# Performance work log

Hardware: AMD Instinct MI355X
Metric: run time of the kernel (lower is better)

## Reference

```python
import jax, jax.numpy as jnp
import numpy as np

B, TV, L = 64, 80, 20
V, H, VD = 10000, 512, 4096
NH = 4  # attention heads


def _lstm_layer(x, wih, whh, bih, bhh):
    # x: [B, T, H_in]; PyTorch gate order i, f, g, o
    b, t = x.shape[0], x.shape[1]
    h_dim = whh.shape[1]
    xg = jnp.einsum('bti,gi->btg', x, wih) + bih + bhh  # [B, T, 4H]

    def step(carry, xg_t):
        h, c = carry
        g = xg_t + h @ whh.T
        i, f, gg, o = jnp.split(g, 4, axis=-1)
        c = jax.nn.sigmoid(f) * c + jax.nn.sigmoid(i) * jnp.tanh(gg)
        h = jax.nn.sigmoid(o) * jnp.tanh(c)
        return (h, c), h

    h0 = jnp.zeros((b, h_dim), x.dtype)
    _, hs = jax.lax.scan(step, (h0, h0), jnp.swapaxes(xg, 0, 1))
    return jnp.swapaxes(hs, 0, 1)


def _lstm2(x, p0, p1):
    # 2-layer LSTM, eval mode (dropout=0.2 between layers is identity at eval)
    return _lstm_layer(_lstm_layer(x, *p0), *p1)


def _mha(q, kv, in_w, in_b, out_w, out_b):
    # torch nn.MultiheadAttention, batch_first, self/cross attention
    h = q.shape[-1]
    d = h // NH
    wq, wk, wv = jnp.split(in_w, 3, axis=0)
    bq, bk, bv = jnp.split(in_b, 3, axis=0)
    Q = (q @ wq.T + bq).reshape(q.shape[0], q.shape[1], NH, d)
    K = (kv @ wk.T + bk).reshape(kv.shape[0], kv.shape[1], NH, d)
    Vv = (kv @ wv.T + bv).reshape(kv.shape[0], kv.shape[1], NH, d)
    scale = jnp.asarray(1.0 / np.sqrt(d), q.dtype)
    scores = jnp.einsum('bqhd,bkhd->bhqk', Q, K) * scale
    attn = jax.nn.softmax(scores, axis=-1)
    out = jnp.einsum('bhqk,bkhd->bqhd', attn, Vv).reshape(q.shape[0], q.shape[1], h)
    return out @ out_w.T + out_b


def setup_inputs() -> dict:
    key = jax.random.key(0)
    ks = iter(jax.random.split(key, 40))
    s = 0.05
    d = {}
    d['video_features'] = jax.random.normal(next(ks), (B, TV, VD), jnp.float32)
    d['captions'] = jax.random.randint(next(ks), (B, L), 0, V, jnp.int64)
    d['vpw'] = jax.random.normal(next(ks), (H, VD), jnp.float32) * s
    d['vpb'] = jnp.zeros((H,), jnp.float32)
    d['emb_table'] = jax.random.normal(next(ks), (V, H), jnp.float32) * s
    for pfx in ['e0', 'e1', 'd0', 'd1']:
        d[pfx + '_wih'] = jax.random.normal(next(ks), (4 * H, H), jnp.float32) * s
        d[pfx + '_whh'] = jax.random.normal(next(ks), (4 * H, H), jnp.float32) * s
        d[pfx + '_bih'] = jnp.zeros((4 * H,), jnp.float32)
        d[pfx + '_bhh'] = jnp.zeros((4 * H,), jnp.float32)
    d['a_inw'] = jax.random.normal(next(ks), (3 * H, H), jnp.float32) * s
    d['a_inb'] = jnp.zeros((3 * H,), jnp.float32)
    d['a_outw'] = jax.random.normal(next(ks), (H, H), jnp.float32) * s
    d['a_outb'] = jnp.zeros((H,), jnp.float32)
    d['ow'] = jax.random.normal(next(ks), (V, H), jnp.float32) * s
    d['ob'] = jnp.zeros((V,), jnp.float32)
    return d


def reference(video_features, captions, vpw, vpb, emb_table,
              e0_wih, e0_whh, e0_bih, e0_bhh, e1_wih, e1_whh, e1_bih, e1_bhh,
              d0_wih, d0_whh, d0_bih, d0_bhh, d1_wih, d1_whh, d1_bih, d1_bhh,
              a_inw, a_inb, a_outw, a_outb, ow, ob):
    # Encoder
    vproj = jnp.einsum('btv,hv->bth', video_features, vpw) + vpb
    enc = _lstm2(vproj, (e0_wih, e0_whh, e0_bih, e0_bhh), (e1_wih, e1_whh, e1_bih, e1_bhh))
    # Decoder (teacher forcing, sampling_prob=0): inputs are captions[:, :-1].
    # Each step's attention query only sees encoder output -> vectorize over steps.
    emb = emb_table[captions[:, :-1]]                      # [B, L-1, H]
    attended = _mha(emb, enc, a_inw, a_inb, a_outw, a_outb)  # [B, L-1, H]
    dec = _lstm2(attended, (d0_wih, d0_whh, d0_bih, d0_bhh), (d1_wih, d1_whh, d1_bih, d1_bhh))
    logits = jnp.einsum('bth,vh->btv', dec, ow) + ob       # [B, L-1, V]
    return logits
```

## Files before the change

### kernel.cpp

```cpp
#include <hip/hip_runtime.h>
#include <hip/hip_bf16.h>
#include <math.h>

typedef unsigned short ushort_t;
typedef __attribute__((ext_vector_type(8))) short short8;
typedef __attribute__((ext_vector_type(4))) float f32x4;

#define B_ 64
#define TV_ 80
#define TD_ 19
#define H_ 512
#define VD_ 4096
#define NV_ 10000
#define G4_ 2048
#define HN_ 32768
#define XN_ 16384

__device__ __forceinline__ float bf2f(ushort_t u) {
  unsigned int x = ((unsigned int)u) << 16;
  float f;
  __builtin_memcpy(&f, &x, 4);
  return f;
}
__device__ __forceinline__ ushort_t f2bf(float f) {
  unsigned int x;
  __builtin_memcpy(&x, &f, 4);
  x = (x + 0x7FFFu + ((x >> 16) & 1u)) >> 16;
  return (ushort_t)x;
}
__device__ __forceinline__ float sigmoidf_(float x) { return 1.0f / (1.0f + expf(-x)); }
__device__ __forceinline__ short8 zero8() {
  short8 z = {0, 0, 0, 0, 0, 0, 0, 0};
  return z;
}
__device__ __forceinline__ short8 cvt_frag(const float* __restrict__ p) {
  float4 v0 = *reinterpret_cast<const float4*>(p);
  float4 v1 = *reinterpret_cast<const float4*>(p + 4);
  short8 r;
  r[0] = (short)f2bf(v0.x); r[1] = (short)f2bf(v0.y);
  r[2] = (short)f2bf(v0.z); r[3] = (short)f2bf(v0.w);
  r[4] = (short)f2bf(v1.x); r[5] = (short)f2bf(v1.y);
  r[6] = (short)f2bf(v1.z); r[7] = (short)f2bf(v1.w);
  return r;
}
__device__ __forceinline__ short8 unpack_hi(uint4 q0, uint4 q1) {
  union { unsigned int u[4]; short8 s; } r;
  r.u[0] = __builtin_amdgcn_perm(q0.y, q0.x, 0x05040100u);
  r.u[1] = __builtin_amdgcn_perm(q0.w, q0.z, 0x05040100u);
  r.u[2] = __builtin_amdgcn_perm(q1.y, q1.x, 0x05040100u);
  r.u[3] = __builtin_amdgcn_perm(q1.w, q1.z, 0x05040100u);
  return r.s;
}
__device__ __forceinline__ short8 unpack_lo(uint4 q0, uint4 q1) {
  union { unsigned int u[4]; short8 s; } r;
  r.u[0] = __builtin_amdgcn_perm(q0.y, q0.x, 0x07060302u);
  r.u[1] = __builtin_amdgcn_perm(q0.w, q0.z, 0x07060302u);
  r.u[2] = __builtin_amdgcn_perm(q1.y, q1.x, 0x07060302u);
  r.u[3] = __builtin_amdgcn_perm(q1.w, q1.z, 0x07060302u);
  return r.s;
}

__global__ __launch_bounds__(256) void cvt_f32_bf16(const float* __restrict__ in,
                                                    ushort_t* __restrict__ outp, int n4) {
  int i = blockIdx.x * 256 + threadIdx.x;
  if (i < n4) {
    float4 v = reinterpret_cast<const float4*>(in)[i];
    ushort4 r;
    r.x = f2bf(v.x); r.y = f2bf(v.y); r.z = f2bf(v.z); r.w = f2bf(v.w);
    reinterpret_cast<ushort4*>(outp)[i] = r;
  }
}

__device__ __forceinline__ void cvt_blk(const float* __restrict__ in,
                                        ushort_t* __restrict__ outp, int local, int tid) {
  int i = local * 256 + tid;
  float4 v = reinterpret_cast<const float4*>(in)[i];
  ushort4 r;
  r.x = f2bf(v.x); r.y = f2bf(v.y); r.z = f2bf(v.z); r.w = f2bf(v.w);
  reinterpret_cast<ushort4*>(outp)[i] = r;
}
__global__ __launch_bounds__(256) void prep_small(
    const float* __restrict__ vpw, ushort_t* __restrict__ vpw_bf,
    const float* __restrict__ wih0, ushort_t* __restrict__ wih0_bf,
    const float* __restrict__ wih2, ushort_t* __restrict__ wih2_bf,
    const float* __restrict__ ainw, ushort_t* __restrict__ ainw_bf,
    const float* __restrict__ aoutw, ushort_t* __restrict__ aoutw_bf,
    const float* __restrict__ ow, ushort_t* __restrict__ ow_bf,
    float* __restrict__ vpf, float* __restrict__ flags, float* __restrict__ ringA0,
    float* __restrict__ ringB0, float* __restrict__ ringX0) {
  int b = (int)blockIdx.x;
  int tid = (int)threadIdx.x;
  if (b < 2048) { cvt_blk(vpw, vpw_bf, b, tid); return; }
  if (b < 3072) { cvt_blk(wih0, wih0_bf, b - 2048, tid); return; }
  if (b < 4096) { cvt_blk(wih2, wih2_bf, b - 3072, tid); return; }
  if (b < 4864) { cvt_blk(ainw, ainw_bf, b - 4096, tid); return; }
  if (b < 5120) { cvt_blk(aoutw, aoutw_bf, b - 4864, tid); return; }
  if (b < 10120) { cvt_blk(ow, ow_bf, b - 5120, tid); return; }
  float4 z = {0.f, 0.f, 0.f, 0.f};
  if (b < 12680) { reinterpret_cast<float4*>(vpf)[(b - 10120) * 256 + tid] = z; return; }
  if (b < 12688) { reinterpret_cast<float4*>(flags)[(b - 12680) * 256 + tid] = z; return; }
  if (b < 12720) { reinterpret_cast<float4*>(ringA0)[(b - 12688) * 256 + tid] = z; return; }
  if (b < 12752) { reinterpret_cast<float4*>(ringB0)[(b - 12720) * 256 + tid] = z; return; }
  reinterpret_cast<float4*>(ringX0)[(b - 12752) * 256 + tid] = z;
}

__global__ __launch_bounds__(64) void prep_weights(
    const float* __restrict__ s0, ushort_t* __restrict__ h0, ushort_t* __restrict__ l0,
    const float* __restrict__ s1, ushort_t* __restrict__ h1, ushort_t* __restrict__ l1,
    const float* __restrict__ s2, ushort_t* __restrict__ h2, ushort_t* __restrict__ l2,
    const float* __restrict__ s3, ushort_t* __restrict__ h3, ushort_t* __restrict__ l3,
    const float* __restrict__ wi1, ushort_t* __restrict__ wd1, const float* __restrict__ wi3,
    ushort_t* __restrict__ wd3, const float* __restrict__ bih1, const float* __restrict__ bhh1,
    float* __restrict__ bc1, const float* __restrict__ bih3, const float* __restrict__ bhh3,
    float* __restrict__ bc3) {
  int y = (int)blockIdx.y;
  int p = (int)blockIdx.x;
  int tid = (int)threadIdx.x;
  if (y == 6) {
    if (p >= 64) return;
    int idx = p * 64 + tid;
    int layer = idx >> 11, q = idx & 2047;
    const float* bih = layer ? bih3 : bih1;
    const float* bhh = layer ? bhh3 : bhh1;
    float* bc = layer ? bc3 : bc1;
    int tile = q >> 4, r = q & 15, gate = r >> 2, sc = r & 3;
    int src = gate * H_ + tile * 4 + sc;
    bc[q] = bih[src] + bhh[src];
    return;
  }
  int tile = p >> 4, r = p & 15, gate = r >> 2, sc = r & 3;
  int i = tid * 8;
  if (y >= 4) {
    const float* src = (y == 4) ? wi1 : wi3;
    ushort_t* hi = (y == 4) ? wd1 : wd3;
    const float* s = src + ((size_t)(gate * H_ + tile * 4 + sc)) * H_;
    float4 v0 = *reinterpret_cast<const float4*>(s + i);
    float4 v1 = *reinterpret_cast<const float4*>(s + i + 4);
    ushort_t* hp = hi + (size_t)p * H_ + i;
    ushort4 rh0, rh1;
    rh0.x = f2bf(v0.x); rh0.y = f2bf(v0.y); rh0.z = f2bf(v0.z); rh0.w = f2bf(v0.w);
    rh1.x = f2bf(v1.x); rh1.y = f2bf(v1.y); rh1.z = f2bf(v1.z); rh1.w = f2bf(v1.w);
    reinterpret_cast<ushort4*>(hp)[0] = rh0;
    reinterpret_cast<ushort4*>(hp)[1] = rh1;
    return;
  }
  const float* src = (y == 0) ? s0 : (y == 1) ? s1 : (y == 2) ? s2 : s3;
  ushort_t* hi = (y == 0) ? h0 : (y == 1) ? h1 : (y == 2) ? h2 : h3;
  ushort_t* lo = (y == 0) ? l0 : (y == 1) ? l1 : (y == 2) ? l2 : l3;
  const float* s = src + ((size_t)(gate * H_ + tile * 4 + sc)) * H_;
  float4 v0 = *reinterpret_cast<const float4*>(s + i);
  float4 v1 = *reinterpret_cast<const float4*>(s + i + 4);
  ushort_t* hp = hi + (size_t)p * H_ + i;
  ushort_t* lp = lo + (size_t)p * H_ + i;
  ushort4 rh0, rl0, rh1, rl1;
  rh0.x = f2bf(v0.x); rl0.x = f2bf(v0.x - bf2f(rh0.x));
  rh0.y = f2bf(v0.y); rl0.y = f2bf(v0.y - bf2f(rh0.y));
  rh0.z = f2bf(v0.z); rl0.z = f2bf(v0.z - bf2f(rh0.z));
  rh0.w = f2bf(v0.w); rl0.w = f2bf(v0.w - bf2f(rh0.w));
  rh1.x = f2bf(v1.x); rl1.x = f2bf(v1.x - bf2f(rh1.x));
  rh1.y = f2bf(v1.y); rl1.y = f2bf(v1.y - bf2f(rh1.y));
  rh1.z = f2bf(v1.z); rl1.z = f2bf(v1.z - bf2f(rh1.z));
  rh1.w = f2bf(v1.w); rl1.w = f2bf(v1.w - bf2f(rh1.w));
  reinterpret_cast<ushort4*>(hp)[0] = rh0;
  reinterpret_cast<ushort4*>(hp)[1] = rh1;
  reinterpret_cast<ushort4*>(lp)[0] = rl0;
  reinterpret_cast<ushort4*>(lp)[1] = rl1;
}

__device__ __forceinline__ void store_c(float* C, size_t idx, float v) { C[idx] = v; }
__device__ __forceinline__ void store_c(ushort_t* C, size_t idx, float v) { C[idx] = f2bf(v); }

template <typename OT>
__global__ __launch_bounds__(256) void gemm_nt_mfma(const ushort_t* __restrict__ A,
                                                    const ushort_t* __restrict__ W,
                                                    const float* __restrict__ bias1,
                                                    const float* __restrict__ bias2,
                                                    OT* __restrict__ C, int M, int N, int K) {
  int tid = threadIdx.x;
  int l = tid & 63, w = tid >> 6;
  int wm = w >> 1, wn = w & 1;
  int row0 = blockIdx.y * 64 + wm * 32;
  int col0 = blockIdx.x * 64 + wn * 32;
  int lr = l & 15;
  int kb = (l >> 4) << 3;
  int ar0 = row0 + lr, ar1 = row0 + 16 + lr;
  int wr0 = col0 + lr, wr1 = col0 + 16 + lr;
  bool aok0 = ar0 < M, aok1 = ar1 < M;
  bool wok0 = wr0 < N, wok1 = wr1 < N;
  f32x4 acc00 = {0.f, 0.f, 0.f, 0.f}, acc01 = acc00, acc10 = acc00, acc11 = acc00;
#pragma unroll 2
  for (int k0 = 0; k0 < K; k0 += 32) {
    int k = k0 + kb;
    short8 a0 = aok0 ? *reinterpret_cast<const short8*>(A + (size_t)ar0 * K + k) : zero8();
    short8 a1 = aok1 ? *reinterpret_cast<const short8*>(A + (size_t)ar1 * K + k) : zero8();
    short8 b0 = wok0 ? *reinterpret_cast<const short8*>(W + (size_t)wr0 * K + k) : zero8();
    short8 b1 = wok1 ? *reinterpret_cast<const short8*>(W + (size_t)wr1 * K + k) : zero8();
    acc00 = __builtin_amdgcn_mfma_f32_16x16x32_bf16(a0, b0, acc00, 0, 0, 0);
    acc01 = __builtin_amdgcn_mfma_f32_16x16x32_bf16(a0, b1, acc01, 0, 0, 0);
    acc10 = __builtin_amdgcn_mfma_f32_16x16x32_bf16(a1, b0, acc10, 0, 0, 0);
    acc11 = __builtin_amdgcn_mfma_f32_16x16x32_bf16(a1, b1, acc11, 0, 0, 0);
  }
  int rb = (l >> 4) << 2;
#pragma unroll
  for (int i = 0; i < 2; ++i) {
#pragma unroll
    for (int v = 0; v < 4; ++v) {
      int r = row0 + i * 16 + rb + v;
      if (r < M) {
#pragma unroll
        for (int j = 0; j < 2; ++j) {
          int cc = col0 + j * 16 + lr;
          if (cc < N) {
            float av;
            if (i == 0) av = (j == 0) ? acc00[v] : acc01[v];
            else        av = (j == 0) ? acc10[v] : acc11[v];
            if (bias1) av += bias1[cc];
            if (bias2) av += bias2[cc];
            store_c(C, (size_t)r * N + cc, av);
          }
        }
      }
    }
  }
}

__global__ __launch_bounds__(256) void gemm_qkv(const int* __restrict__ cap,
                                                const float* __restrict__ emb_table,
                                                const ushort_t* __restrict__ hse1,
                                                const ushort_t* __restrict__ ainw,
                                                const float* __restrict__ ainb,
                                                float* __restrict__ Qf, float* __restrict__ Kf,
                                                float* __restrict__ Vf) {
  int z = blockIdx.z;
  if (z == 0 && blockIdx.y >= 19) return;
  const ushort_t* W = ainw + (size_t)z * H_ * H_;
  const float* bias = ainb + z * H_;
  float* C = (z == 0) ? Qf : ((z == 1) ? Kf : Vf);
  int tid = threadIdx.x;
  int l = tid & 63, w = tid >> 6;
  int wm = w >> 1, wn = w & 1;
  int row0 = blockIdx.y * 64 + wm * 32;
  int col0 = blockIdx.x * 64 + wn * 32;
  int lr = l & 15;
  int kb = (l >> 4) << 3;
  int ar0 = row0 + lr, ar1 = row0 + 16 + lr;
  const ushort_t* b0p = W + (size_t)(col0 + lr) * H_ + kb;
  const ushort_t* b1p = W + (size_t)(col0 + 16 + lr) * H_ + kb;
  f32x4 acc00 = {0.f, 0.f, 0.f, 0.f}, acc01 = acc00, acc10 = acc00, acc11 = acc00;
  if (z == 0) {
    int b0 = ar0 / TD_, t0 = ar0 - b0 * TD_;
    int b1 = ar1 / TD_, t1 = ar1 - b1 * TD_;
    const float* a0base = emb_table + (size_t)cap[b0 * 20 + t0] * H_ + kb;
    const float* a1base = emb_table + (size_t)cap[b1 * 20 + t1] * H_ + kb;
#pragma unroll 2
    for (int k0 = 0; k0 < H_; k0 += 32) {
      short8 a0 = cvt_frag(a0base + k0);
      short8 a1 = cvt_frag(a1base + k0);
      short8 bb0 = *reinterpret_cast<const short8*>(b0p + k0);
      short8 bb1 = *reinterpret_cast<const short8*>(b1p + k0);
      acc00 = __builtin_amdgcn_mfma_f32_16x16x32_bf16(a0, bb0, acc00, 0, 0, 0);
      acc01 = __builtin_amdgcn_mfma_f32_16x16x32_bf16(a0, bb1, acc01, 0, 0, 0);
      acc10 = __builtin_amdgcn_mfma_f32_16x16x32_bf16(a1, bb0, acc10, 0, 0, 0);
      acc11 = __builtin_amdgcn_mfma_f32_16x16x32_bf16(a1, bb1, acc11, 0, 0, 0);
    }
  } else {
    const ushort_t* a0p = hse1 + (size_t)ar0 * H_ + kb;
    const ushort_t* a1p = hse1 + (size_t)ar1 * H_ + kb;
#pragma unroll 2
    for (int k0 = 0; k0 < H_; k0 += 32) {
      short8 a0 = *reinterpret_cast<const short8*>(a0p + k0);
      short8 a1 = *reinterpret_cast<const short8*>(a1p + k0);
      short8 bb0 = *reinterpret_cast<const short8*>(b0p + k0);
      short8 bb1 = *reinterpret_cast<const short8*>(b1p + k0);
      acc00 = __builtin_amdgcn_mfma_f32_16x16x32_bf16(a0, bb0, acc00, 0, 0, 0);
      acc01 = __builtin_amdgcn_mfma_f32_16x16x32_bf16(a0, bb1, acc01, 0, 0, 0);
      acc10 = __builtin_amdgcn_mfma_f32_16x16x32_bf16(a1, bb0, acc10, 0, 0, 0);
      acc11 = __builtin_amdgcn_mfma_f32_16x16x32_bf16(a1, bb1, acc11, 0, 0, 0);
    }
  }
  int rb = (l >> 4) << 2;
#pragma unroll
  for (int i = 0; i < 2; ++i)
#pragma unroll
    for (int v = 0; v < 4; ++v) {
      int r = row0 + i * 16 + rb + v;
#pragma unroll
      for (int j = 0; j < 2; ++j) {
        int cc = col0 + j * 16 + lr;
        float av;
        if (i == 0) av = (j == 0) ? acc00[v] : acc01[v];
        else        av = (j == 0) ? acc10[v] : acc11[v];
        C[(size_t)r * H_ + cc] = av + bias[cc];
      }
    }
}

template <typename OT>
__global__ __launch_bounds__(256) void gemm_nt_big(const ushort_t* __restrict__ A,
                                                   const ushort_t* __restrict__ W,
                                                   const float* __restrict__ bias1,
                                                   const float* __restrict__ bias2,
                                                   OT* __restrict__ C, int M, int N, int K) {
  int tid = threadIdx.x;
  int l = tid & 63, w = tid >> 6;
  int row0 = blockIdx.y * 64;
  int col0 = blockIdx.x * 256 + w * 64;
  int lr = l & 15, kb = (l >> 4) << 3;
  f32x4 acc[4][4];
#pragma unroll
  for (int i = 0; i < 4; ++i)
#pragma unroll
    for (int j = 0; j < 4; ++j) acc[i][j] = (f32x4){0.f, 0.f, 0.f, 0.f};
  const ushort_t* aps[4];
  const ushort_t* wps[4];
  bool wok[4];
#pragma unroll
  for (int fi = 0; fi < 4; ++fi) aps[fi] = A + (size_t)(row0 + fi * 16 + lr) * K + kb;
#pragma unroll
  for (int fj = 0; fj < 4; ++fj) {
    int wr = col0 + fj * 16 + lr;
    wok[fj] = wr < N;
    wps[fj] = W + (size_t)(wok[fj] ? wr : 0) * K + kb;
  }
#pragma unroll 2
  for (int k0 = 0; k0 < K; k0 += 32) {
    short8 af[4], bf[4];
#pragma unroll
    for (int fi = 0; fi < 4; ++fi) af[fi] = *reinterpret_cast<const short8*>(aps[fi] + k0);
#pragma unroll
    for (int fj = 0; fj < 4; ++fj)
      bf[fj] = wok[fj] ? *reinterpret_cast<const short8*>(wps[fj] + k0) : zero8();
#pragma unroll
    for (int fi = 0; fi < 4; ++fi)
#pragma unroll
      for (int fj = 0; fj < 4; ++fj)
        acc[fi][fj] = __builtin_amdgcn_mfma_f32_16x16x32_bf16(af[fi], bf[fj], acc[fi][fj], 0, 0, 0);
  }
  int rb = (l >> 4) << 2;
#pragma unroll
  for (int fi = 0; fi < 4; ++fi) {
#pragma unroll
    for (int v = 0; v < 4; ++v) {
      int r = row0 + fi * 16 + rb + v;
#pragma unroll
      for (int fj = 0; fj < 4; ++fj) {
        int cc = col0 + fj * 16 + lr;
        if (cc < N) {
          float av = acc[fi][fj][v];
          if (bias1) av += bias1[cc];
          if (bias2) av += bias2[cc];
          store_c(C, (size_t)r * N + cc, av);
        }
      }
    }
  }
}

__global__ __launch_bounds__(256) void gemm_nt_big_split(const ushort_t* __restrict__ A,
                                                         const ushort_t* __restrict__ W,
                                                         float* __restrict__ C, int M, int N,
                                                         int K, int kc) {
  int tid = threadIdx.x;
  int l = tid & 63, w = tid >> 6;
  int row0 = blockIdx.y * 64;
  int col0 = blockIdx.x * 256 + w * 64;
  int lr = l & 15, kb = (l >> 4) << 3;
  int kbeg = blockIdx.z * kc;
  f32x4 acc[4][4];
#pragma unroll
  for (int i = 0; i < 4; ++i)
#pragma unroll
    for (int j = 0; j < 4; ++j) acc[i][j] = (f32x4){0.f, 0.f, 0.f, 0.f};
  const ushort_t* aps[4];
  const ushort_t* wps[4];
#pragma unroll
  for (int fi = 0; fi < 4; ++fi)
    aps[fi] = A + (size_t)(row0 + fi * 16 + lr) * K + kbeg + kb;
#pragma unroll
  for (int fj = 0; fj < 4; ++fj)
    wps[fj] = W + (size_t)(col0 + fj * 16 + lr) * K + kbeg + kb;
#pragma unroll 2
  for (int k0 = 0; k0 < kc; k0 += 32) {
    short8 af[4], bf[4];
#pragma unroll
    for (int fi = 0; fi < 4; ++fi) af[fi] = *reinterpret_cast<const short8*>(aps[fi] + k0);
#pragma unroll
    for (int fj = 0; fj < 4; ++fj) bf[fj] = *reinterpret_cast<const short8*>(wps[fj] + k0);
#pragma unroll
    for (int fi = 0; fi < 4; ++fi)
#pragma unroll
      for (int fj = 0; fj < 4; ++fj)
        acc[fi][fj] = __builtin_amdgcn_mfma_f32_16x16x32_bf16(af[fi], bf[fj], acc[fi][fj], 0, 0, 0);
  }
  int rb = (l >> 4) << 2;
#pragma unroll
  for (int fi = 0; fi < 4; ++fi)
#pragma unroll
    for (int v = 0; v < 4; ++v) {
      int r = row0 + fi * 16 + rb + v;
#pragma unroll
      for (int fj = 0; fj < 4; ++fj) {
        int cc = col0 + fj * 16 + lr;
        atomicAdd(&C[(size_t)r * N + cc], acc[fi][fj][v]);
      }
    }
}

__global__ __launch_bounds__(256) void bias_cvt_bf16(const float* __restrict__ in,
                                                     const float* __restrict__ bias,
                                                     ushort_t* __restrict__ outp, int ncols,
                                                     int n4) {
  int i = blockIdx.x * 256 + threadIdx.x;
  if (i < n4) {
    float4 v = reinterpret_cast<const float4*>(in)[i];
    int col = (i * 4) & (ncols - 1);
    float4 bv = *reinterpret_cast<const float4*>(bias + col);
    ushort4 r;
    r.x = f2bf(v.x + bv.x); r.y = f2bf(v.y + bv.y);
    r.z = f2bf(v.z + bv.z); r.w = f2bf(v.w + bv.w);
    reinterpret_cast<ushort4*>(outp)[i] = r;
  }
}

__device__ __forceinline__ void wait_flags2(const int* __restrict__ fA, int tA,
                                            const int* __restrict__ fB, int tB, int tid) {
  if (tid < 64) {
    for (;;) {
      int a0 = __hip_atomic_load(fA + tid * 16, __ATOMIC_RELAXED, __HIP_MEMORY_SCOPE_AGENT);
      int a1 = __hip_atomic_load(fA + (tid + 64) * 16, __ATOMIC_RELAXED, __HIP_MEMORY_SCOPE_AGENT);
      bool ok = (a0 >= tA) && (a1 >= tA);
      if (fB) {
        int b0 = __hip_atomic_load(fB + tid * 16, __ATOMIC_RELAXED, __HIP_MEMORY_SCOPE_AGENT);
        int b1 = __hip_atomic_load(fB + (tid + 64) * 16, __ATOMIC_RELAXED, __HIP_MEMORY_SCOPE_AGENT);
        ok = ok && (b0 >= tB) && (b1 >= tB);
      }
      if (__all(ok)) break;
      __builtin_amdgcn_s_sleep(2);
    }
  }
  __syncthreads();
}

__global__ __launch_bounds__(512, 2) void lstm_ring(
    const float* __restrict__ xg, const ushort_t* __restrict__ whhA_hi,
    const ushort_t* __restrict__ whhA_lo, const ushort_t* __restrict__ whhB_hi,
    const ushort_t* __restrict__ whhB_lo, const ushort_t* __restrict__ wihB,
    const float* __restrict__ bcB, unsigned int* __restrict__ ringA,
    unsigned int* __restrict__ ringB, unsigned int* __restrict__ ringX,
    ushort_t* __restrict__ hsB, int T, int* __restrict__ flagA, int* __restrict__ flagB) {
  __shared__ float gbuf[2][64][17];
  const int role = (int)(blockIdx.x >> 7);
  const int tile = (int)(blockIdx.x & 127);
  const int tid = (int)threadIdx.x;
  const int g2 = tid >> 8;
  const int u = tid & 255;
  const int l = u & 63, w = u >> 6;
  const int lr = l & 15, kq = l >> 4;
  const int kb = g2 * 256 + (kq << 3);
  const int arow = (w << 4) + lr;
  const int prow = tile * 16 + lr;
  const int row = tid >> 2, s = tid & 3;
  const int col = (tile << 2) + s;
  unsigned int* ring_own = role ? ringB : ringA;
  int* flag_own = (role ? flagB : flagA) + tile * 16;

  short8 wb[8], wbl[8];
  {
    const ushort_t* bp = (role ? whhB_hi : whhA_hi) + (size_t)prow * H_ + kb;
    const ushort_t* blp = (role ? whhB_lo : whhA_lo) + (size_t)prow * H_ + kb;
#pragma unroll
    for (int i = 0; i < 8; ++i) {
      wb[i] = *reinterpret_cast<const short8*>(bp + i * 32);
      wbl[i] = *reinterpret_cast<const short8*>(blp + i * 32);
    }
  }
  const ushort_t* wpp = wihB + (size_t)prow * H_ + kb;
  float bci = 0.f, bcf = 0.f, bcg = 0.f, bco = 0.f;
  if (role && tid < 256) {
    bci = bcB[tile * 16 + 0 + s];
    bcf = bcB[tile * 16 + 4 + s];
    bcg = bcB[tile * 16 + 8 + s];
    bco = bcB[tile * 16 + 12 + s];
  }
  float creg = 0.f;
  for (int t = 0; t < T; ++t) {
    float xgi = 0.f, xgf = 0.f, xgg = 0.f, xgo = 0.f;
    if (!role && tid < 256) {
      size_t xb = ((size_t)row * T + t) * (size_t)G4_ + col;
      xgi = xg[xb]; xgf = xg[xb + 512]; xgg = xg[xb + 1024]; xgo = xg[xb + 1536];
    }
    if (role == 0) {
      if (t > 0) wait_flags2(flagA, t, nullptr, 0, tid);
      else __syncthreads();
    } else {
      wait_flags2(flagA, t + 1, (t > 0) ? flagB : nullptr, t, tid);
    }
    const unsigned int* rh = ring_own + (size_t)t * HN_ + (size_t)arow * H_ + kb;
    f32x4 a0 = {0.f, 0.f, 0.f, 0.f}, a1 = a0, a2 = a0, a3 = a0;
    if (role == 0) {
      uint4 q[16];
#pragma unroll
      for (int i = 0; i < 8; ++i) {
        q[2 * i] = *reinterpret_cast<const uint4*>(rh + i * 32);
        q[2 * i + 1] = *reinterpret_cast<const uint4*>(rh + i * 32 + 4);
      }
#pragma unroll
      for (int i = 0; i < 8; ++i) {
        short8 a = unpack_hi(q[2 * i], q[2 * i + 1]);
        short8 al = unpack_lo(q[2 * i], q[2 * i + 1]);
        a0 = __builtin_amdgcn_mfma_f32_16x16x32_bf16(a, wb[i], a0, 0, 0, 0);
        a1 = __builtin_amdgcn_mfma_f32_16x16x32_bf16(al, wb[i], a1, 0, 0, 0);
        a2 = __builtin_amdgcn_mfma_f32_16x16x32_bf16(a, wbl[i], a2, 0, 0, 0);
      }
    } else {
      const unsigned int* rxp =
          ringX + (size_t)(t + 1) * XN_ + (size_t)arow * 256 + (kb >> 1);
      uint4 q[16], x[8];
#pragma unroll
      for (int i = 0; i < 8; ++i) {
        q[2 * i] = *reinterpret_cast<const uint4*>(rh + i * 32);
        q[2 * i + 1] = *reinterpret_cast<const uint4*>(rh + i * 32 + 4);
      }
#pragma unroll
      for (int i = 0; i < 8; ++i) x[i] = *reinterpret_cast<const uint4*>(rxp + i * 16);
#pragma unroll
      for (int i = 0; i < 8; ++i) {
        short8 a = unpack_hi(q[2 * i], q[2 * i + 1]);
        short8 al = unpack_lo(q[2 * i], q[2 * i + 1]);
        union { uint4 u; short8 s8; } xv;
        xv.u = x[i];
        short8 wx = *reinterpret_cast<const short8*>(wpp + i * 32);
        a0 = __builtin_amdgcn_mfma_f32_16x16x32_bf16(a, wb[i], a0, 0, 0, 0);
        a1 = __builtin_amdgcn_mfma_f32_16x16x32_bf16(al, wb[i], a1, 0, 0, 0);
        a2 = __builtin_amdgcn_mfma_f32_16x16x32_bf16(a, wbl[i], a2, 0, 0, 0);
        a3 = __builtin_amdgcn_mfma_f32_16x16x32_bf16(xv.s8, wx, a3, 0, 0, 0);
      }
    }
    f32x4 acc = (a0 + a1) + (a2 + a3);
    const int rb = (w << 4) + (kq << 2);
#pragma unroll
    for (int v = 0; v < 4; ++v) gbuf[g2][rb + v][lr] = acc[v];
    __syncthreads();
    if (tid < 256) {
      float gi = gbuf[0][row][0 + s] + gbuf[1][row][0 + s];
      float gf = gbuf[0][row][4 + s] + gbuf[1][row][4 + s];
      float gg = gbuf[0][row][8 + s] + gbuf[1][row][8 + s];
      float go = gbuf[0][row][12 + s] + gbuf[1][row][12 + s];
      if (role) {
        gi += bci; gf += bcf; gg += bcg; go += bco;
      } else {
        gi += xgi; gf += xgf; gg += xgg; go += xgo;
      }
      float cv = sigmoidf_(gf) * creg + sigmoidf_(gi) * tanhf(gg);
      float hv = sigmoidf_(go) * tanhf(cv);
      creg = cv;
      ushort_t hh = f2bf(hv);
      ushort_t hl = f2bf(hv - bf2f(hh));
      unsigned int pk = (unsigned int)hh | ((unsigned int)hl << 16);
      __hip_atomic_store(ring_own + (size_t)(t + 1) * HN_ + (size_t)row * H_ + col, pk,
                         __ATOMIC_RELAXED, __HIP_MEMORY_SCOPE_AGENT);
      if (role == 0) {
        unsigned int hu = (unsigned int)hh;
        unsigned int hpair = hu | (((unsigned int)__shfl_down(hu, 1)) << 16);
        if ((s & 1) == 0)
          __hip_atomic_store(ringX + (size_t)(t + 1) * XN_ + (size_t)row * 256 + (col >> 1),
                             hpair, __ATOMIC_RELAXED, __HIP_MEMORY_SCOPE_AGENT);
      } else {
        hsB[((size_t)row * T + t) * H_ + col] = hh;
      }
    }
    __syncthreads();
    if (tid == 0)
      __hip_atomic_store(flag_own, t + 1, __ATOMIC_RELAXED, __HIP_MEMORY_SCOPE_AGENT);
  }
}

__global__ __launch_bounds__(256) void mha_kernel(const float* __restrict__ Qf,
                                                  const float* __restrict__ Kf,
                                                  const float* __restrict__ Vf,
                                                  ushort_t* __restrict__ attnout) {
  __shared__ float Qs[19][132];
  __shared__ float Ks[80][132];
  __shared__ float Ss[19][80];
  int h = blockIdx.x, b = blockIdx.y;
  int tid = threadIdx.x;
  for (int idx = tid; idx < 19 * 128; idx += 256) {
    int q = idx >> 7, d = idx & 127;
    Qs[q][d] = Qf[((size_t)(b * TD_ + q)) * H_ + h * 128 + d];
  }
  for (int idx = tid; idx < 80 * 128; idx += 256) {
    int k = idx >> 7, d = idx & 127;
    Ks[k][d] = Kf[((size_t)(b * TV_ + k)) * H_ + h * 128 + d];
  }
  __syncthreads();
  for (int u = tid; u < 240; u += 256) {
    int k = u / 3, qo = u % 3;
    int q0 = qo * 8;
    int nq = (qo == 2) ? 3 : 8;
    float s[8] = {0.f, 0.f, 0.f, 0.f, 0.f, 0.f, 0.f, 0.f};
    for (int d = 0; d < 128; d += 4) {
      float4 kv = *reinterpret_cast<const float4*>(&Ks[k][d]);
#pragma unroll
      for (int qi = 0; qi < 8; ++qi) {
        if (qi < nq) {
          float4 qv = *reinterpret_cast<const float4*>(&Qs[q0 + qi][d]);
          s[qi] += qv.x * kv.x + qv.y * kv.y + qv.z * kv.z + qv.w * kv.w;
        }
      }
    }
    for (int qi = 0; qi < nq; ++qi) Ss[q0 + qi][k] = s[qi] * 0.08838834764831845f;
  }
  __syncthreads();
  if (tid < 19) {
    float m = -1e30f;
    for (int k = 0; k < 80; ++k) m = fmaxf(m, Ss[tid][k]);
    float sum = 0.f;
    for (int k = 0; k < 80; ++k) {
      float e = expf(Ss[tid][k] - m);
      Ss[tid][k] = e;
      sum += e;
    }
    float inv = 1.0f / sum;
    for (int k = 0; k < 80; ++k) Ss[tid][k] *= inv;
  }
  __syncthreads();
  for (int u = tid; u < 160; u += 256) {
    int qp = u / 16, d0 = (u % 16) * 8;
    int q0 = qp * 2;
    int nq = (q0 + 1 < 19) ? 2 : 1;
    float o0[8] = {0.f, 0.f, 0.f, 0.f, 0.f, 0.f, 0.f, 0.f};
    float o1[8] = {0.f, 0.f, 0.f, 0.f, 0.f, 0.f, 0.f, 0.f};
#pragma unroll 4
    for (int k = 0; k < 80; ++k) {
      const float* vp = Vf + ((size_t)(b * TV_ + k)) * H_ + h * 128 + d0;
      float4 v0 = *reinterpret_cast<const float4*>(vp);
      float4 v1 = *reinterpret_cast<const float4*>(vp + 4);
      float p0 = Ss[q0][k];
      o0[0] += p0 * v0.x; o0[1] += p0 * v0.y; o0[2] += p0 * v0.z; o0[3] += p0 * v0.w;
      o0[4] += p0 * v1.x; o0[5] += p0 * v1.y; o0[6] += p0 * v1.z; o0[7] += p0 * v1.w;
      if (nq == 2) {
        float p1 = Ss[q0 + 1][k];
        o1[0] += p1 * v0.x; o1[1] += p1 * v0.y; o1[2] += p1 * v0.z; o1[3] += p1 * v0.w;
        o1[4] += p1 * v1.x; o1[5] += p1 * v1.y; o1[6] += p1 * v1.z; o1[7] += p1 * v1.w;
      }
    }
    for (int j = 0; j < 8; ++j)
      attnout[((size_t)(b * TD_ + q0)) * H_ + h * 128 + d0 + j] = f2bf(o0[j]);
    if (nq == 2)
      for (int j = 0; j < 8; ++j)
        attnout[((size_t)(b * TD_ + q0 + 1)) * H_ + h * 128 + d0 + j] = f2bf(o1[j]);
  }
}

extern "C" void kernel_launch(void* const* d_in, const int* in_sizes, int n_in, void* d_out,
                              int out_size, void* d_ws, size_t ws_size, hipStream_t stream) {
  const float* video = (const float*)d_in[0];
  const int* captions = (const int*)d_in[1];
  const float* vpw = (const float*)d_in[2];
  const float* vpb = (const float*)d_in[3];
  const float* emb_table = (const float*)d_in[4];
  const float* wih[4] = {(const float*)d_in[5], (const float*)d_in[9], (const float*)d_in[13],
                         (const float*)d_in[17]};
  const float* whh[4] = {(const float*)d_in[6], (const float*)d_in[10], (const float*)d_in[14],
                         (const float*)d_in[18]};
  const float* bih[4] = {(const float*)d_in[7], (const float*)d_in[11], (const float*)d_in[15],
                         (const float*)d_in[19]};
  const float* bhh[4] = {(const float*)d_in[8], (const float*)d_in[12], (const float*)d_in[16],
                         (const float*)d_in[20]};
  const float* a_inw = (const float*)d_in[21];
  const float* a_inb = (const float*)d_in[22];
  const float* a_outw = (const float*)d_in[23];
  const float* a_outb = (const float*)d_in[24];
  const float* ow = (const float*)d_in[25];
  const float* ob = (const float*)d_in[26];
  float* out = (float*)d_out;

  char* ws = (char*)d_ws;
  size_t o = 0;
  auto take = [&](size_t bytes) {
    size_t cur = o;
    o += (bytes + 255) & ~(size_t)255;
    return cur;
  };
  const size_t o_vpw = take((size_t)H_ * VD_ * 2);
  size_t o_wih_std[4], o_whhp_hi[4], o_whhp_lo[4], o_wihp[4], o_bc[4];
  for (int i = 0; i < 4; ++i) {
    o_wih_std[i] = (i == 0 || i == 2) ? take((size_t)G4_ * H_ * 2) : 0;
    o_whhp_hi[i] = take((size_t)G4_ * H_ * 2);
    o_whhp_lo[i] = take((size_t)G4_ * H_ * 2);
    o_wihp[i] = (i == 1 || i == 3) ? take((size_t)G4_ * H_ * 2) : 0;
    o_bc[i] = (i == 1 || i == 3) ? take((size_t)G4_ * 4) : 0;
  }
  const size_t o_ainw = take((size_t)3 * H_ * H_ * 2);
  const size_t o_aoutw = take((size_t)H_ * H_ * 2);
  const size_t o_ow = take((size_t)NV_ * H_ * 2);
  const size_t o_vproj = take((size_t)B_ * TV_ * H_ * 2);
  const size_t o_xg = take((size_t)B_ * TV_ * G4_ * 4);
  const size_t o_hse1 = take((size_t)B_ * TV_ * H_ * 2);
  const size_t o_attn = take((size_t)B_ * TD_ * H_ * 2);
  const size_t o_attd = take((size_t)B_ * TD_ * H_ * 2);
  const size_t o_hsd1 = take((size_t)B_ * TD_ * H_ * 2);
  const size_t o_flags = take(4 * 128 * 64);
  const size_t o_vpf = take((size_t)B_ * TV_ * H_ * 4);
  const size_t o_ringA = take((size_t)(TV_ + 1) * HN_ * 4);
  const size_t o_ringB = take((size_t)(TV_ + 1) * HN_ * 4);
  const size_t o_ringX = take((size_t)(TV_ + 1) * XN_ * 4);

  ushort_t* vpw_bf = (ushort_t*)(ws + o_vpw);
  ushort_t* ainw_bf = (ushort_t*)(ws + o_ainw);
  ushort_t* aoutw_bf = (ushort_t*)(ws + o_aoutw);
  ushort_t* ow_bf = (ushort_t*)(ws + o_ow);
  ushort_t* vproj_bf = (ushort_t*)(ws + o_vproj);
  float* xg = (float*)(ws + o_xg);
  ushort_t* video_bf = (ushort_t*)(ws + o_xg);
  ushort_t* hse1 = (ushort_t*)(ws + o_hse1);
  ushort_t* attn_bf = (ushort_t*)(ws + o_attn);
  ushort_t* attd_bf = (ushort_t*)(ws + o_attd);
  ushort_t* hsd1 = (ushort_t*)(ws + o_hsd1);
  float* Qf = (float*)(ws + o_xg);
  float* Kf = (float*)(ws + o_xg + 2490368);
  float* Vf = (float*)(ws + o_xg + 2490368 + 10485760);
  int* flagA0 = (int*)(ws + o_flags);
  int* flagB0 = flagA0 + 2048;
  int* flagA1 = flagA0 + 4096;
  int* flagB1 = flagA0 + 6144;
  float* vpf = (float*)(ws + o_vpf);
  unsigned int* ringA = (unsigned int*)(ws + o_ringA);
  unsigned int* ringB = (unsigned int*)(ws + o_ringB);
  unsigned int* ringX = (unsigned int*)(ws + o_ringX);

  cvt_f32_bf16<<<dim3(20480), dim3(256), 0, stream>>>(video, video_bf,
                                                      (int)((size_t)B_ * TV_ * VD_ / 4));
  prep_small<<<dim3(12768), dim3(256), 0, stream>>>(
      vpw, vpw_bf, wih[0], (ushort_t*)(ws + o_wih_std[0]), wih[2],
      (ushort_t*)(ws + o_wih_std[2]), a_inw, ainw_bf, a_outw, aoutw_bf, ow, ow_bf, vpf,
      (float*)(ws + o_flags), (float*)ringA, (float*)ringB, (float*)ringX);
  prep_weights<<<dim3(G4_, 7), dim3(64), 0, stream>>>(
      whh[0], (ushort_t*)(ws + o_whhp_hi[0]), (ushort_t*)(ws + o_whhp_lo[0]), whh[1],
      (ushort_t*)(ws + o_whhp_hi[1]), (ushort_t*)(ws + o_whhp_lo[1]), whh[2],
      (ushort_t*)(ws + o_whhp_hi[2]), (ushort_t*)(ws + o_whhp_lo[2]), whh[3],
      (ushort_t*)(ws + o_whhp_hi[3]), (ushort_t*)(ws + o_whhp_lo[3]), wih[1],
      (ushort_t*)(ws + o_wihp[1]), wih[3], (ushort_t*)(ws + o_wihp[3]), bih[1], bhh[1],
      (float*)(ws + o_bc[1]), bih[3], bhh[3], (float*)(ws + o_bc[3]));

  gemm_nt_big_split<<<dim3(2, 80, 4), dim3(256), 0, stream>>>(video_bf, vpw_bf, vpf, B_ * TV_,
                                                              H_, VD_, VD_ / 4);
  bias_cvt_bf16<<<dim3((B_ * TV_ * H_ / 4 + 255) / 256), dim3(256), 0, stream>>>(
      vpf, vpb, vproj_bf, H_, B_ * TV_ * H_ / 4);

  gemm_nt_big<float><<<dim3(8, 80), dim3(256), 0, stream>>>(
      vproj_bf, (const ushort_t*)(ws + o_wih_std[0]), bih[0], bhh[0], xg, B_ * TV_, G4_, H_);

  lstm_ring<<<dim3(256), dim3(512), 0, stream>>>(
      xg, (const ushort_t*)(ws + o_whhp_hi[0]), (const ushort_t*)(ws + o_whhp_lo[0]),
      (const ushort_t*)(ws + o_whhp_hi[1]), (const ushort_t*)(ws + o_whhp_lo[1]),
      (const ushort_t*)(ws + o_wihp[1]), (const float*)(ws + o_bc[1]), ringA, ringB, ringX,
      hse1, TV_, flagA0, flagB0);

  gemm_qkv<<<dim3(8, 80, 3), dim3(256), 0, stream>>>(captions, emb_table, hse1, ainw_bf, a_inb,
                                                     Qf, Kf, Vf);

  mha_kernel<<<dim3(4, B_), dim3(256), 0, stream>>>(Qf, Kf, Vf, attn_bf);

  gemm_nt_mfma<ushort_t><<<dim3(8, TD_), dim3(256), 0, stream>>>(
      attn_bf, aoutw_bf, a_outb, nullptr, attd_bf, B_ * TD_, H_, H_);
  gemm_nt_big<float><<<dim3(8, TD_), dim3(256), 0, stream>>>(
      attd_bf, (const ushort_t*)(ws + o_wih_std[2]), bih[2], bhh[2], xg, B_ * TD_, G4_, H_);

  lstm_ring<<<dim3(256), dim3(512), 0, stream>>>(
      xg, (const ushort_t*)(ws + o_whhp_hi[2]), (const ushort_t*)(ws + o_whhp_lo[2]),
      (const ushort_t*)(ws + o_whhp_hi[3]), (const ushort_t*)(ws + o_whhp_lo[3]),
      (const ushort_t*)(ws + o_wihp[3]), (const float*)(ws + o_bc[3]), ringA, ringB, ringX,
      hsd1, TD_, flagA1, flagB1);

  gemm_nt_big<float><<<dim3((NV_ + 255) / 256, TD_), dim3(256), 0, stream>>>(
      hsd1, ow_bf, ob, nullptr, out, B_ * TD_, NV_, H_);
}
```

Before: 1.314 ms.

## Fuse layer-0 input projection into the LSTM ring kernel and merge video conversion

```diff
diff --git a/kernel.cpp b/kernel.cpp
--- a/kernel.cpp
+++ b/kernel.cpp
@@ -60,17 +60,6 @@
   return r.s;
 }
 
-__global__ __launch_bounds__(256) void cvt_f32_bf16(const float* __restrict__ in,
-                                                    ushort_t* __restrict__ outp, int n4) {
-  int i = blockIdx.x * 256 + threadIdx.x;
-  if (i < n4) {
-    float4 v = reinterpret_cast<const float4*>(in)[i];
-    ushort4 r;
-    r.x = f2bf(v.x); r.y = f2bf(v.y); r.z = f2bf(v.z); r.w = f2bf(v.w);
-    reinterpret_cast<ushort4*>(outp)[i] = r;
-  }
-}
-
 __device__ __forceinline__ void cvt_blk(const float* __restrict__ in,
                                         ushort_t* __restrict__ outp, int local, int tid) {
   int i = local * 256 + tid;
@@ -80,9 +69,8 @@
   reinterpret_cast<ushort4*>(outp)[i] = r;
 }
 __global__ __launch_bounds__(256) void prep_small(
+    const float* __restrict__ video, ushort_t* __restrict__ video_bf,
     const float* __restrict__ vpw, ushort_t* __restrict__ vpw_bf,
-    const float* __restrict__ wih0, ushort_t* __restrict__ wih0_bf,
-    const float* __restrict__ wih2, ushort_t* __restrict__ wih2_bf,
     const float* __restrict__ ainw, ushort_t* __restrict__ ainw_bf,
     const float* __restrict__ aoutw, ushort_t* __restrict__ aoutw_bf,
     const float* __restrict__ ow, ushort_t* __restrict__ ow_bf,
@@ -90,18 +78,17 @@
     float* __restrict__ ringB0, float* __restrict__ ringX0) {
   int b = (int)blockIdx.x;
   int tid = (int)threadIdx.x;
-  if (b < 2048) { cvt_blk(vpw, vpw_bf, b, tid); return; }
-  if (b < 3072) { cvt_blk(wih0, wih0_bf, b - 2048, tid); return; }
-  if (b < 4096) { cvt_blk(wih2, wih2_bf, b - 3072, tid); return; }
-  if (b < 4864) { cvt_blk(ainw, ainw_bf, b - 4096, tid); return; }
-  if (b < 5120) { cvt_blk(aoutw, aoutw_bf, b - 4864, tid); return; }
-  if (b < 10120) { cvt_blk(ow, ow_bf, b - 5120, tid); return; }
+  if (b < 20480) { cvt_blk(video, video_bf, b, tid); return; }
+  if (b < 22528) { cvt_blk(vpw, vpw_bf, b - 20480, tid); return; }
+  if (b < 23296) { cvt_blk(ainw, ainw_bf, b - 22528, tid); return; }
+  if (b < 23552) { cvt_blk(aoutw, aoutw_bf, b - 23296, tid); return; }
+  if (b < 28552) { cvt_blk(ow, ow_bf, b - 23552, tid); return; }
   float4 z = {0.f, 0.f, 0.f, 0.f};
-  if (b < 12680) { reinterpret_cast<float4*>(vpf)[(b - 10120) * 256 + tid] = z; return; }
-  if (b < 12688) { reinterpret_cast<float4*>(flags)[(b - 12680) * 256 + tid] = z; return; }
-  if (b < 12720) { reinterpret_cast<float4*>(ringA0)[(b - 12688) * 256 + tid] = z; return; }
-  if (b < 12752) { reinterpret_cast<float4*>(ringB0)[(b - 12720) * 256 + tid] = z; return; }
-  reinterpret_cast<float4*>(ringX0)[(b - 12752) * 256 + tid] = z;
+  if (b < 31112) { reinterpret_cast<float4*>(vpf)[(b - 28552) * 256 + tid] = z; return; }
+  if (b < 31120) { reinterpret_cast<float4*>(flags)[(b - 31112) * 256 + tid] = z; return; }
+  if (b < 31152) { reinterpret_cast<float4*>(ringA0)[(b - 31120) * 256 + tid] = z; return; }
+  if (b < 31184) { reinterpret_cast<float4*>(ringB0)[(b - 31152) * 256 + tid] = z; return; }
+  reinterpret_cast<float4*>(ringX0)[(b - 31184) * 256 + tid] = z;
 }
 
 __global__ __launch_bounds__(64) void prep_weights(
@@ -109,20 +96,23 @@
     const float* __restrict__ s1, ushort_t* __restrict__ h1, ushort_t* __restrict__ l1,
     const float* __restrict__ s2, ushort_t* __restrict__ h2, ushort_t* __restrict__ l2,
     const float* __restrict__ s3, ushort_t* __restrict__ h3, ushort_t* __restrict__ l3,
-    const float* __restrict__ wi1, ushort_t* __restrict__ wd1, const float* __restrict__ wi3,
-    ushort_t* __restrict__ wd3, const float* __restrict__ bih1, const float* __restrict__ bhh1,
-    float* __restrict__ bc1, const float* __restrict__ bih3, const float* __restrict__ bhh3,
-    float* __restrict__ bc3) {
+    const float* __restrict__ wi0, ushort_t* __restrict__ wd0, const float* __restrict__ wi1,
+    ushort_t* __restrict__ wd1, const float* __restrict__ wi2, ushort_t* __restrict__ wd2,
+    const float* __restrict__ wi3, ushort_t* __restrict__ wd3,
+    const float* __restrict__ bih0, const float* __restrict__ bhh0, float* __restrict__ bc0,
+    const float* __restrict__ bih1, const float* __restrict__ bhh1, float* __restrict__ bc1,
+    const float* __restrict__ bih2, const float* __restrict__ bhh2, float* __restrict__ bc2,
+    const float* __restrict__ bih3, const float* __restrict__ bhh3, float* __restrict__ bc3) {
   int y = (int)blockIdx.y;
   int p = (int)blockIdx.x;
   int tid = (int)threadIdx.x;
-  if (y == 6) {
-    if (p >= 64) return;
+  if (y == 8) {
+    if (p >= 128) return;
     int idx = p * 64 + tid;
     int layer = idx >> 11, q = idx & 2047;
-    const float* bih = layer ? bih3 : bih1;
-    const float* bhh = layer ? bhh3 : bhh1;
-    float* bc = layer ? bc3 : bc1;
+    const float* bih = (layer == 0) ? bih0 : (layer == 1) ? bih1 : (layer == 2) ? bih2 : bih3;
+    const float* bhh = (layer == 0) ? bhh0 : (layer == 1) ? bhh1 : (layer == 2) ? bhh2 : bhh3;
+    float* bc = (layer == 0) ? bc0 : (layer == 1) ? bc1 : (layer == 2) ? bc2 : bc3;
     int tile = q >> 4, r = q & 15, gate = r >> 2, sc = r & 3;
     int src = gate * H_ + tile * 4 + sc;
     bc[q] = bih[src] + bhh[src];
@@ -131,8 +121,9 @@
   int tile = p >> 4, r = p & 15, gate = r >> 2, sc = r & 3;
   int i = tid * 8;
   if (y >= 4) {
-    const float* src = (y == 4) ? wi1 : wi3;
-    ushort_t* hi = (y == 4) ? wd1 : wd3;
+    int ly = y - 4;
+    const float* src = (ly == 0) ? wi0 : (ly == 1) ? wi1 : (ly == 2) ? wi2 : wi3;
+    ushort_t* hi = (ly == 0) ? wd0 : (ly == 1) ? wd1 : (ly == 2) ? wd2 : wd3;
     const float* s = src + ((size_t)(gate * H_ + tile * 4 + sc)) * H_;
     float4 v0 = *reinterpret_cast<const float4*>(s + i);
     float4 v1 = *reinterpret_cast<const float4*>(s + i + 4);
@@ -442,7 +433,8 @@
 }
 
 __global__ __launch_bounds__(512, 2) void lstm_ring(
-    const float* __restrict__ xg, const ushort_t* __restrict__ whhA_hi,
+    const ushort_t* __restrict__ xsrcA, const ushort_t* __restrict__ wihA,
+    const float* __restrict__ bcA, const ushort_t* __restrict__ whhA_hi,
     const ushort_t* __restrict__ whhA_lo, const ushort_t* __restrict__ whhB_hi,
     const ushort_t* __restrict__ whhB_lo, const ushort_t* __restrict__ wihB,
     const float* __restrict__ bcB, unsigned int* __restrict__ ringA,
@@ -474,21 +466,17 @@
       wbl[i] = *reinterpret_cast<const short8*>(blp + i * 32);
     }
   }
-  const ushort_t* wpp = wihB + (size_t)prow * H_ + kb;
+  const ushort_t* wpp = (role ? wihB : wihA) + (size_t)prow * H_ + kb;
   float bci = 0.f, bcf = 0.f, bcg = 0.f, bco = 0.f;
-  if (role && tid < 256) {
-    bci = bcB[tile * 16 + 0 + s];
-    bcf = bcB[tile * 16 + 4 + s];
-    bcg = bcB[tile * 16 + 8 + s];
-    bco = bcB[tile * 16 + 12 + s];
+  if (tid < 256) {
+    const float* bc = role ? bcB : bcA;
+    bci = bc[tile * 16 + 0 + s];
+    bcf = bc[tile * 16 + 4 + s];
+    bcg = bc[tile * 16 + 8 + s];
+    bco = bc[tile * 16 + 12 + s];
   }
   float creg = 0.f;
   for (int t = 0; t < T; ++t) {
-    float xgi = 0.f, xgf = 0.f, xgg = 0.f, xgo = 0.f;
-    if (!role && tid < 256) {
-      size_t xb = ((size_t)row * T + t) * (size_t)G4_ + col;
-      xgi = xg[xb]; xgf = xg[xb + 512]; xgg = xg[xb + 1024]; xgo = xg[xb + 1536];
-    }
     if (role == 0) {
       if (t > 0) wait_flags2(flagA, t, nullptr, 0, tid);
       else __syncthreads();
@@ -498,6 +486,7 @@
     const unsigned int* rh = ring_own + (size_t)t * HN_ + (size_t)arow * H_ + kb;
     f32x4 a0 = {0.f, 0.f, 0.f, 0.f}, a1 = a0, a2 = a0, a3 = a0;
     if (role == 0) {
+      const ushort_t* xp = xsrcA + ((size_t)arow * T + t) * H_ + kb;
       uint4 q[16];
 #pragma unroll
       for (int i = 0; i < 8; ++i) {
@@ -508,9 +497,12 @@
       for (int i = 0; i < 8; ++i) {
         short8 a = unpack_hi(q[2 * i], q[2 * i + 1]);
         short8 al = unpack_lo(q[2 * i], q[2 * i + 1]);
+        short8 xf = *reinterpret_cast<const short8*>(xp + i * 32);
+        short8 wx = *reinterpret_cast<const short8*>(wpp + i * 32);
         a0 = __builtin_amdgcn_mfma_f32_16x16x32_bf16(a, wb[i], a0, 0, 0, 0);
         a1 = __builtin_amdgcn_mfma_f32_16x16x32_bf16(al, wb[i], a1, 0, 0, 0);
         a2 = __builtin_amdgcn_mfma_f32_16x16x32_bf16(a, wbl[i], a2, 0, 0, 0);
+        a3 = __builtin_amdgcn_mfma_f32_16x16x32_bf16(xf, wx, a3, 0, 0, 0);
       }
     } else {
       const unsigned int* rxp =
@@ -542,15 +534,10 @@
     for (int v = 0; v < 4; ++v) gbuf[g2][rb + v][lr] = acc[v];
     __syncthreads();
     if (tid < 256) {
-      float gi = gbuf[0][row][0 + s] + gbuf[1][row][0 + s];
-      float gf = gbuf[0][row][4 + s] + gbuf[1][row][4 + s];
-      float gg = gbuf[0][row][8 + s] + gbuf[1][row][8 + s];
-      float go = gbuf[0][row][12 + s] + gbuf[1][row][12 + s];
-      if (role) {
-        gi += bci; gf += bcf; gg += bcg; go += bco;
-      } else {
-        gi += xgi; gf += xgf; gg += xgg; go += xgo;
-      }
+      float gi = gbuf[0][row][0 + s] + gbuf[1][row][0 + s] + bci;
+      float gf = gbuf[0][row][4 + s] + gbuf[1][row][4 + s] + bcf;
+      float gg = gbuf[0][row][8 + s] + gbuf[1][row][8 + s] + bcg;
+      float go = gbuf[0][row][12 + s] + gbuf[1][row][12 + s] + bco;
       float cv = sigmoidf_(gf) * creg + sigmoidf_(gi) * tanhf(gg);
       float hv = sigmoidf_(go) * tanhf(cv);
       creg = cv;
@@ -683,13 +670,12 @@
     return cur;
   };
   const size_t o_vpw = take((size_t)H_ * VD_ * 2);
-  size_t o_wih_std[4], o_whhp_hi[4], o_whhp_lo[4], o_wihp[4], o_bc[4];
+  size_t o_whhp_hi[4], o_whhp_lo[4], o_wihp[4], o_bc[4];
   for (int i = 0; i < 4; ++i) {
-    o_wih_std[i] = (i == 0 || i == 2) ? take((size_t)G4_ * H_ * 2) : 0;
     o_whhp_hi[i] = take((size_t)G4_ * H_ * 2);
     o_whhp_lo[i] = take((size_t)G4_ * H_ * 2);
-    o_wihp[i] = (i == 1 || i == 3) ? take((size_t)G4_ * H_ * 2) : 0;
-    o_bc[i] = (i == 1 || i == 3) ? take((size_t)G4_ * 4) : 0;
+    o_wihp[i] = take((size_t)G4_ * H_ * 2);
+    o_bc[i] = take((size_t)G4_ * 4);
   }
   const size_t o_ainw = take((size_t)3 * H_ * H_ * 2);
   const size_t o_aoutw = take((size_t)H_ * H_ * 2);
@@ -711,7 +697,6 @@
   ushort_t* aoutw_bf = (ushort_t*)(ws + o_aoutw);
   ushort_t* ow_bf = (ushort_t*)(ws + o_ow);
   ushort_t* vproj_bf = (ushort_t*)(ws + o_vproj);
-  float* xg = (float*)(ws + o_xg);
   ushort_t* video_bf = (ushort_t*)(ws + o_xg);
   ushort_t* hse1 = (ushort_t*)(ws + o_hse1);
   ushort_t* attn_bf = (ushort_t*)(ws + o_attn);
@@ -729,30 +714,27 @@
   unsigned int* ringB = (unsigned int*)(ws + o_ringB);
   unsigned int* ringX = (unsigned int*)(ws + o_ringX);
 
-  cvt_f32_bf16<<<dim3(20480), dim3(256), 0, stream>>>(video, video_bf,
-                                                      (int)((size_t)B_ * TV_ * VD_ / 4));
-  prep_small<<<dim3(12768), dim3(256), 0, stream>>>(
-      vpw, vpw_bf, wih[0], (ushort_t*)(ws + o_wih_std[0]), wih[2],
-      (ushort_t*)(ws + o_wih_std[2]), a_inw, ainw_bf, a_outw, aoutw_bf, ow, ow_bf, vpf,
+  prep_small<<<dim3(31200), dim3(256), 0, stream>>>(
+      video, video_bf, vpw, vpw_bf, a_inw, ainw_bf, a_outw, aoutw_bf, ow, ow_bf, vpf,
       (float*)(ws + o_flags), (float*)ringA, (float*)ringB, (float*)ringX);
-  prep_weights<<<dim3(G4_, 7), dim3(64), 0, stream>>>(
+  prep_weights<<<dim3(G4_, 9), dim3(64), 0, stream>>>(
       whh[0], (ushort_t*)(ws + o_whhp_hi[0]), (ushort_t*)(ws + o_whhp_lo[0]), whh[1],
       (ushort_t*)(ws + o_whhp_hi[1]), (ushort_t*)(ws + o_whhp_lo[1]), whh[2],
       (ushort_t*)(ws + o_whhp_hi[2]), (ushort_t*)(ws + o_whhp_lo[2]), whh[3],
-      (ushort_t*)(ws + o_whhp_hi[3]), (ushort_t*)(ws + o_whhp_lo[3]), wih[1],
-      (ushort_t*)(ws + o_wihp[1]), wih[3], (ushort_t*)(ws + o_wihp[3]), bih[1], bhh[1],
-      (float*)(ws + o_bc[1]), bih[3], bhh[3], (float*)(ws + o_bc[3]));
+      (ushort_t*)(ws + o_whhp_hi[3]), (ushort_t*)(ws + o_whhp_lo[3]),
+      wih[0], (ushort_t*)(ws + o_wihp[0]), wih[1], (ushort_t*)(ws + o_wihp[1]),
+      wih[2], (ushort_t*)(ws + o_wihp[2]), wih[3], (ushort_t*)(ws + o_wihp[3]),
+      bih[0], bhh[0], (float*)(ws + o_bc[0]), bih[1], bhh[1], (float*)(ws + o_bc[1]),
+      bih[2], bhh[2], (float*)(ws + o_bc[2]), bih[3], bhh[3], (float*)(ws + o_bc[3]));
 
   gemm_nt_big_split<<<dim3(2, 80, 4), dim3(256), 0, stream>>>(video_bf, vpw_bf, vpf, B_ * TV_,
                                                               H_, VD_, VD_ / 4);
   bias_cvt_bf16<<<dim3((B_ * TV_ * H_ / 4 + 255) / 256), dim3(256), 0, stream>>>(
       vpf, vpb, vproj_bf, H_, B_ * TV_ * H_ / 4);
 
-  gemm_nt_big<float><<<dim3(8, 80), dim3(256), 0, stream>>>(
-      vproj_bf, (const ushort_t*)(ws + o_wih_std[0]), bih[0], bhh[0], xg, B_ * TV_, G4_, H_);
-
   lstm_ring<<<dim3(256), dim3(512), 0, stream>>>(
-      xg, (const ushort_t*)(ws + o_whhp_hi[0]), (const ushort_t*)(ws + o_whhp_lo[0]),
+      vproj_bf, (const ushort_t*)(ws + o_wihp[0]), (const float*)(ws + o_bc[0]),
+      (const ushort_t*)(ws + o_whhp_hi[0]), (const ushort_t*)(ws + o_whhp_lo[0]),
       (const ushort_t*)(ws + o_whhp_hi[1]), (const ushort_t*)(ws + o_whhp_lo[1]),
       (const ushort_t*)(ws + o_wihp[1]), (const float*)(ws + o_bc[1]), ringA, ringB, ringX,
       hse1, TV_, flagA0, flagB0);
@@ -764,11 +746,10 @@
 
   gemm_nt_mfma<ushort_t><<<dim3(8, TD_), dim3(256), 0, stream>>>(
       attn_bf, aoutw_bf, a_outb, nullptr, attd_bf, B_ * TD_, H_, H_);
-  gemm_nt_big<float><<<dim3(8, TD_), dim3(256), 0, stream>>>(
-      attd_bf, (const ushort_t*)(ws + o_wih_std[2]), bih[2], bhh[2], xg, B_ * TD_, G4_, H_);
 
   lstm_ring<<<dim3(256), dim3(512), 0, stream>>>(
-      xg, (const ushort_t*)(ws + o_whhp_hi[2]), (const ushort_t*)(ws + o_whhp_lo[2]),
+      attd_bf, (const ushort_t*)(ws + o_wihp[2]), (const float*)(ws + o_bc[2]),
+      (const ushort_t*)(ws + o_whhp_hi[2]), (const ushort_t*)(ws + o_whhp_lo[2]),
       (const ushort_t*)(ws + o_whhp_hi[3]), (const ushort_t*)(ws + o_whhp_lo[3]),
       (const ushort_t*)(ws + o_wihp[3]), (const float*)(ws + o_bc[3]), ringA, ringB, ringX,
       hsd1, TD_, flagA1, flagB1);
```

Result: faster. 1.234 ms (-6.1%).
